# Kernel tuning notes

Hardware: AMD Instinct MI355X
Metric: run time of the kernel (lower is better)

Reference implementation:

```python
import jax, jax.numpy as jnp
import numpy as np
import math
from jax import lax

L = 16
T = 2 ** 14          # hash table size (power of 2 -> uint32 arithmetic is exact mod T)
F_DIM = 2
N_MIN, N_MAX = 16, 512
_B = math.exp((math.log(N_MAX) - math.log(N_MIN)) / (L - 1))
NS = [int(N_MIN * _B ** i) for i in range(L)]
PRIME = np.uint32(2654435761)


def setup_inputs() -> dict:
    key = jax.random.key(0)
    k1, k2 = jax.random.split(key)
    x = jax.random.uniform(k1, (8, 2, 512, 512), dtype=jnp.float32)
    hash_table = jax.random.uniform(k2, (L, T, F_DIM), dtype=jnp.float32) * 2e-4 - 1e-4
    return {"x": x, "hash_table": hash_table}


def reference(x, hash_table):
    b, c, h, w = x.shape
    feats = []
    for i, n in enumerate(NS):
        kh, kw = h // n, w // n
        # max_pool2d(x*n, (kh,kw), stride=1) -> [b, 2, h-kh+1, w-kw+1]
        g = lax.reduce_window(x * n, -jnp.inf, lax.max,
                              (1, 1, kh, kw), (1, 1, 1, 1), 'VALID')
        g = g.astype(jnp.uint32)  # trunc toward zero, values nonneg and small
        # prime-XOR hash; T is a power of two so uint32 wraparound matches int64 math mod T
        idx = (g[:, 0] ^ (g[:, 1] * PRIME)) % np.uint32(T)  # [b, gh, gw]
        f = hash_table[i][idx]                 # gather -> [b, gh, gw, F_DIM]
        f = jnp.transpose(f, (0, 3, 1, 2))     # [b, F_DIM, gh, gw]
        # bilinear upsample (half-pixel centers == align_corners=False)
        f = jax.image.resize(f, (b, F_DIM, h, w), method='bilinear')
        feats.append(f)
    return jnp.concatenate(feats, axis=1)       # [b, L*F_DIM, h, w]
```

## Files before the change

kernel.cpp:

```cpp
#include <hip/hip_runtime.h>
#include <stdint.h>

#define NLVL 16
#define TSIZE 16384
#define HW 512

typedef float vfloat4 __attribute__((ext_vector_type(4)));

__constant__ int c_n[NLVL] = {16,20,25,32,40,50,64,80,101,128,161,203,256,322,406,512};

__device__ __forceinline__ uint32_t pkmax(uint32_t a, uint32_t b) {
    uint32_t r;
    asm("v_pk_max_u16 %0, %1, %2" : "=v"(r) : "v"(a), "v"(b));
    return r;
}

template<int K>
__device__ __forceinline__ void do_tile(
        const int lvl, const int b, const int tx0, const int ty0,
        const float* __restrict__ x, const float* __restrict__ table,
        float* __restrict__ out, uint32_t* lds) {
    constexpr int gh = 513 - K;
    constexpr float s = (float)gh * (1.0f / 512.0f);
    const float nf = (float)c_n[lvl];
    const int tid = threadIdx.x;

    const float* xb0 = x + (size_t)b * 2 * HW * HW;
    const float* xb1 = xb0 + HW * HW;
    const float2* tb = (const float2*)table + (size_t)lvl * TSIZE;
    float* ob = out + ((size_t)b * 32 + lvl * 2) * HW * HW;

    uint32_t* V   = lds;
    float2*  feat = (float2*)(lds + 33 * 68);

    const int gy_base = (int)floorf(((float)ty0 + 0.5f) * s - 0.5f);
    const int gx_base = (int)floorf(((float)tx0 + 0.5f) * s - 0.5f);
    const int rmin = max(gy_base, 0);
    const int cmin = max(gx_base, 0);

    {
        const int wv = __builtin_amdgcn_readfirstlane(tid >> 6);
        const int c  = tid & 63;
        const int r0 = 8 * wv;
        const int xx = min(cmin + c, HW - 1);
        const int ybase = rmin + r0;
        uint32_t e[K + 8];
#pragma unroll
        for (int t = 0; t < K + 8; ++t) {
            const int yy = min(ybase + t, HW - 1);
            const float v0 = (xb0 + yy * HW)[xx];
            const float v1 = (xb1 + yy * HW)[xx];
            e[t] = (uint32_t)(v0 * nf) | ((uint32_t)(v1 * nf) << 16);
        }
        uint32_t o[9];
        if constexpr (K >= 10) {
            uint32_t sfx[9];
            sfx[8] = e[8];
#pragma unroll
            for (int t = 7; t >= 0; --t) sfx[t] = pkmax(e[t], sfx[t + 1]);
            uint32_t run = e[9];
#pragma unroll
            for (int m = 9; m <= K + 7; ++m) {
                if (m > 9) run = pkmax(run, e[m]);
                if (m >= K - 1) o[m - K + 1] = pkmax(sfx[m - K + 1], run);
            }
        } else {
#pragma unroll
            for (int i = 0; i < 9; ++i) {
                uint32_t m = e[i];
#pragma unroll
                for (int t = 1; t < K; ++t) m = pkmax(m, e[i + t]);
                o[i] = m;
            }
        }
        const int vb = r0 * 68 + c;
#pragma unroll
        for (int t = 0; t < 9; ++t) V[vb + t * 68] = o[t];
    }
    __syncthreads();

    if (tid < 99) {
        const int i = tid / 3, g = tid % 3;
        constexpr int NE  = 12 + K - 1;
        constexpr int NCH = (NE + 3) >> 2;
        uint32_t f[NCH * 4];
        const uint4* rp = (const uint4*)(V + i * 68 + 12 * g);
#pragma unroll
        for (int cc = 0; cc < NCH; ++cc) {
            const uint4 q = rp[cc];
            f[4*cc] = q.x; f[4*cc+1] = q.y; f[4*cc+2] = q.z; f[4*cc+3] = q.w;
        }
        uint32_t wm[12];
        if constexpr (K >= 13) {
            uint32_t sfx[12];
            sfx[11] = f[11];
#pragma unroll
            for (int d = 10; d >= 0; --d) sfx[d] = pkmax(f[d], sfx[d + 1]);
            uint32_t run = f[12];
#pragma unroll
            for (int m = 12; m <= K + 10; ++m) {
                if (m > 12) run = pkmax(run, f[m]);
                if (m >= K - 1) wm[m - K + 1] = pkmax(sfx[m - K + 1], run);
            }
        } else {
#pragma unroll
            for (int d = 0; d < 12; ++d) {
                uint32_t m = f[d];
#pragma unroll
                for (int t = 1; t < K; ++t) m = pkmax(m, f[d + t]);
                wm[d] = m;
            }
        }
#pragma unroll
        for (int d = 0; d < 12; ++d) {
            const int j = 12 * g + d;
            if (j < 33) {
                const uint32_t m = wm[d];
                const uint32_t idx = ((m & 0xFFFFu) ^ ((m >> 16) * 2654435761u)) & (TSIZE - 1);
                feat[i * 34 + j] = tb[idx];
            }
        }
    }
    __syncthreads();

    const int bty = tid >> 5, btx = tid & 31;
    const int xo = tx0 + btx;
    const float sxf = ((float)xo + 0.5f) * s - 0.5f;
    const float fxf = floorf(sxf);
    const float wx = sxf - fxf;
    const int x0i = (int)fxf;
    const int jx0 = min(max(x0i, 0), gh - 1) - cmin;
    const int jx1 = min(max(x0i + 1, 0), gh - 1) - cmin;
    for (int oy = bty; oy < 32; oy += 8) {
        const int y = ty0 + oy;
        const float syf = ((float)y + 0.5f) * s - 0.5f;
        const float fyf = floorf(syf);
        const float wy = syf - fyf;
        const int y0i = (int)fyf;
        const int iy0 = min(max(y0i, 0), gh - 1) - rmin;
        const int iy1 = min(max(y0i + 1, 0), gh - 1) - rmin;
        const float2 f00 = feat[iy0 * 34 + jx0], f01 = feat[iy0 * 34 + jx1];
        const float2 f10 = feat[iy1 * 34 + jx0], f11 = feat[iy1 * 34 + jx1];
        const float w11 = wy * wx;
        const float w10 = wy - w11;
        const float w01 = wx - w11;
        const float w00 = 1.0f - wy - wx + w11;
        const float c0 = f00.x * w00 + f01.x * w01 + f10.x * w10 + f11.x * w11;
        const float c1 = f00.y * w00 + f01.y * w01 + f10.y * w10 + f11.y * w11;
        const size_t o = (size_t)y * HW + xo;
        __builtin_nontemporal_store(c0, &ob[o]);
        __builtin_nontemporal_store(c1, &ob[o + (size_t)HW * HW]);
    }
}

__device__ __forceinline__ void identity3(
        const int b, const int tx0, const int ty0,
        const float* __restrict__ x, const float* __restrict__ table,
        float* __restrict__ out) {
    const int tid = threadIdx.x;
    const int oy = tid >> 3, xo = tx0 + (tid & 7) * 4;
    const int y = ty0 + oy;
    const float* xb0 = x + (size_t)b * 2 * HW * HW;
    const float* xb1 = xb0 + HW * HW;
    const float4 v0 = *(const float4*)&xb0[y * HW + xo];
    const float4 v1 = *(const float4*)&xb1[y * HW + xo];
    const size_t o = (size_t)y * HW + xo;
#pragma unroll
    for (int li = 0; li < 3; ++li) {
        const int lvl = 13 + li;
        const float nf = (float)c_n[13 + li];
        const float2* tb = (const float2*)table + (size_t)lvl * TSIZE;
        float* ob = out + ((size_t)b * 32 + lvl * 2) * HW * HW;
        const uint32_t i0 = (((uint32_t)(v0.x * nf)) ^ (((uint32_t)(v1.x * nf)) * 2654435761u)) & (TSIZE - 1);
        const uint32_t i1 = (((uint32_t)(v0.y * nf)) ^ (((uint32_t)(v1.y * nf)) * 2654435761u)) & (TSIZE - 1);
        const uint32_t i2 = (((uint32_t)(v0.z * nf)) ^ (((uint32_t)(v1.z * nf)) * 2654435761u)) & (TSIZE - 1);
        const uint32_t i3 = (((uint32_t)(v0.w * nf)) ^ (((uint32_t)(v1.w * nf)) * 2654435761u)) & (TSIZE - 1);
        const float2 f0 = tb[i0], f1 = tb[i1], f2 = tb[i2], f3 = tb[i3];
        const vfloat4 o0 = (vfloat4){f0.x, f1.x, f2.x, f3.x};
        const vfloat4 o1 = (vfloat4){f0.y, f1.y, f2.y, f3.y};
        __builtin_nontemporal_store(o0, (vfloat4*)&ob[o]);
        __builtin_nontemporal_store(o1, (vfloat4*)&ob[o + (size_t)HW * HW]);
    }
}

__global__ __launch_bounds__(256) void fused_kernel(
        const float* __restrict__ x, const float* __restrict__ table,
        float* __restrict__ out) {
    __shared__ __align__(16) uint32_t lds[33 * 68 + 33 * 34 * 2];

    const int bid  = blockIdx.x;
    const int b    = bid & 7;
    const int tile = (bid >> 3) & 255;
    const int grp  = bid >> 11;
    const int tx0  = (tile & 15) * 32;
    const int ty0  = (tile >> 4) * 32;

    switch (grp) {
        case 0: do_tile<32>( 0, b, tx0, ty0, x, table, out, lds);
                do_tile<25>( 1, b, tx0, ty0, x, table, out, lds); break;
        case 1: do_tile<20>( 2, b, tx0, ty0, x, table, out, lds);
                do_tile<16>( 3, b, tx0, ty0, x, table, out, lds); break;
        case 2: do_tile<12>( 4, b, tx0, ty0, x, table, out, lds);
                do_tile<10>( 5, b, tx0, ty0, x, table, out, lds); break;
        case 3: do_tile< 8>( 6, b, tx0, ty0, x, table, out, lds);
                do_tile< 6>( 7, b, tx0, ty0, x, table, out, lds); break;
        case 4: do_tile< 5>( 8, b, tx0, ty0, x, table, out, lds);
                do_tile< 4>( 9, b, tx0, ty0, x, table, out, lds); break;
        case 5: do_tile< 3>(10, b, tx0, ty0, x, table, out, lds);
                do_tile< 2>(11, b, tx0, ty0, x, table, out, lds); break;
        case 6: do_tile< 2>(12, b, tx0, ty0, x, table, out, lds); break;
        default: identity3(b, tx0, ty0, x, table, out); break;
    }
}

extern "C" void kernel_launch(void* const* d_in, const int* in_sizes, int n_in,
                              void* d_out, int out_size, void* d_ws, size_t ws_size,
                              hipStream_t stream) {
    const float* x     = (const float*)d_in[0];
    const float* table = (const float*)d_in[1];
    float* out         = (float*)d_out;
    (void)d_ws; (void)ws_size;

    fused_kernel<<<dim3(8 * 256 * 8), dim3(256), 0, stream>>>(x, table, out);
}
```

Baseline: 111.7 us.

## Share input column loads between paired pyramid levels in one pass

Paired levels now read the input column strip once and quantize it at both scales, computing the vertical window max for both levels from the same registers. The second level's partial results go into a separate LDS buffer, offset by the row and column difference between the two levels' tile origins. This removes a second pass of global loads per pair. In exchange it uses more registers (two element arrays, extra outputs) and more LDS, which may lower occupancy.

```diff
diff --git a/kernel.cpp b/kernel.cpp
--- a/kernel.cpp
+++ b/kernel.cpp
@@ -15,70 +15,36 @@
     return r;
 }
 
+template<int KK, int P, int NE>
+__device__ __forceinline__ void winmaxNU(const uint32_t (&e)[NE], uint32_t (&o)[P]) {
+    static_assert(NE >= P + KK - 1, "window overrun");
+    if constexpr (KK > P) {
+        uint32_t sfx[P];
+        sfx[P - 1] = e[P - 1];
+#pragma unroll
+        for (int t = P - 2; t >= 0; --t) sfx[t] = pkmax(e[t], sfx[t + 1]);
+        uint32_t run = e[P];
+#pragma unroll
+        for (int m = P; m <= P + KK - 2; ++m) {
+            if (m > P) run = pkmax(run, e[m]);
+            const int j = m - KK + 1;
+            if (j >= 0 && j < P) o[j] = pkmax(sfx[j], run);
+        }
+    } else {
+#pragma unroll
+        for (int i = 0; i < P; ++i) {
+            uint32_t m = e[i];
+#pragma unroll
+            for (int t = 1; t < KK; ++t) m = pkmax(m, e[i + t]);
+            o[i] = m;
+        }
+    }
+}
+
 template<int K>
-__device__ __forceinline__ void do_tile(
-        const int lvl, const int b, const int tx0, const int ty0,
-        const float* __restrict__ x, const float* __restrict__ table,
-        float* __restrict__ out, uint32_t* lds) {
-    constexpr int gh = 513 - K;
-    constexpr float s = (float)gh * (1.0f / 512.0f);
-    const float nf = (float)c_n[lvl];
-    const int tid = threadIdx.x;
-
-    const float* xb0 = x + (size_t)b * 2 * HW * HW;
-    const float* xb1 = xb0 + HW * HW;
-    const float2* tb = (const float2*)table + (size_t)lvl * TSIZE;
-    float* ob = out + ((size_t)b * 32 + lvl * 2) * HW * HW;
-
-    uint32_t* V   = lds;
-    float2*  feat = (float2*)(lds + 33 * 68);
-
-    const int gy_base = (int)floorf(((float)ty0 + 0.5f) * s - 0.5f);
-    const int gx_base = (int)floorf(((float)tx0 + 0.5f) * s - 0.5f);
-    const int rmin = max(gy_base, 0);
-    const int cmin = max(gx_base, 0);
-
-    {
-        const int wv = __builtin_amdgcn_readfirstlane(tid >> 6);
-        const int c  = tid & 63;
-        const int r0 = 8 * wv;
-        const int xx = min(cmin + c, HW - 1);
-        const int ybase = rmin + r0;
-        uint32_t e[K + 8];
-#pragma unroll
-        for (int t = 0; t < K + 8; ++t) {
-            const int yy = min(ybase + t, HW - 1);
-            const float v0 = (xb0 + yy * HW)[xx];
-            const float v1 = (xb1 + yy * HW)[xx];
-            e[t] = (uint32_t)(v0 * nf) | ((uint32_t)(v1 * nf) << 16);
-        }
-        uint32_t o[9];
-        if constexpr (K >= 10) {
-            uint32_t sfx[9];
-            sfx[8] = e[8];
-#pragma unroll
-            for (int t = 7; t >= 0; --t) sfx[t] = pkmax(e[t], sfx[t + 1]);
-            uint32_t run = e[9];
-#pragma unroll
-            for (int m = 9; m <= K + 7; ++m) {
-                if (m > 9) run = pkmax(run, e[m]);
-                if (m >= K - 1) o[m - K + 1] = pkmax(sfx[m - K + 1], run);
-            }
-        } else {
-#pragma unroll
-            for (int i = 0; i < 9; ++i) {
-                uint32_t m = e[i];
-#pragma unroll
-                for (int t = 1; t < K; ++t) m = pkmax(m, e[i + t]);
-                o[i] = m;
-            }
-        }
-        const int vb = r0 * 68 + c;
-#pragma unroll
-        for (int t = 0; t < 9; ++t) V[vb + t * 68] = o[t];
-    }
-    __syncthreads();
-
+__device__ __forceinline__ void phaseB(const uint32_t* __restrict__ V,
+                                       float2* __restrict__ feat,
+                                       const float2* __restrict__ tb, const int tid) {
     if (tid < 99) {
         const int i = tid / 3, g = tid % 3;
         constexpr int NE  = 12 + K - 1;
@@ -91,26 +57,7 @@
             f[4*cc] = q.x; f[4*cc+1] = q.y; f[4*cc+2] = q.z; f[4*cc+3] = q.w;
         }
         uint32_t wm[12];
-        if constexpr (K >= 13) {
-            uint32_t sfx[12];
-            sfx[11] = f[11];
-#pragma unroll
-            for (int d = 10; d >= 0; --d) sfx[d] = pkmax(f[d], sfx[d + 1]);
-            uint32_t run = f[12];
-#pragma unroll
-            for (int m = 12; m <= K + 10; ++m) {
-                if (m > 12) run = pkmax(run, f[m]);
-                if (m >= K - 1) wm[m - K + 1] = pkmax(sfx[m - K + 1], run);
-            }
-        } else {
-#pragma unroll
-            for (int d = 0; d < 12; ++d) {
-                uint32_t m = f[d];
-#pragma unroll
-                for (int t = 1; t < K; ++t) m = pkmax(m, f[d + t]);
-                wm[d] = m;
-            }
-        }
+        winmaxNU<K, 12, NCH * 4>(f, wm);
 #pragma unroll
         for (int d = 0; d < 12; ++d) {
             const int j = 12 * g + d;
@@ -121,8 +68,15 @@
             }
         }
     }
-    __syncthreads();
-
+}
+
+template<int K>
+__device__ __forceinline__ void phaseC(const float2* __restrict__ feat,
+                                       float* __restrict__ ob,
+                                       const int rmin, const int cmin,
+                                       const int tx0, const int ty0, const int tid) {
+    constexpr int gh = 513 - K;
+    constexpr float s = (float)gh * (1.0f / 512.0f);
     const int bty = tid >> 5, btx = tid & 31;
     const int xo = tx0 + btx;
     const float sxf = ((float)xo + 0.5f) * s - 0.5f;
@@ -153,6 +107,114 @@
     }
 }
 
+template<int K1, int K2>
+__device__ __forceinline__ void do_pair(
+        const int l1, const int l2, const int b, const int tx0, const int ty0,
+        const float* __restrict__ x, const float* __restrict__ table,
+        float* __restrict__ out, uint32_t* lds) {
+    constexpr float s1 = (float)(513 - K1) * (1.0f / 512.0f);
+    constexpr float s2 = (float)(513 - K2) * (1.0f / 512.0f);
+    const float nf1 = (float)c_n[l1], nf2 = (float)c_n[l2];
+    const int tid = threadIdx.x;
+
+    const float* xb0 = x + (size_t)b * 2 * HW * HW;
+    const float* xb1 = xb0 + HW * HW;
+
+    uint32_t* V1  = lds;
+    uint32_t* V2  = lds + 2244;
+    float2*  feat = (float2*)(lds + 4488);
+
+    const int rmin1 = max((int)floorf(((float)ty0 + 0.5f) * s1 - 0.5f), 0);
+    const int cmin1 = max((int)floorf(((float)tx0 + 0.5f) * s1 - 0.5f), 0);
+    const int rmin2 = max((int)floorf(((float)ty0 + 0.5f) * s2 - 0.5f), 0);
+    const int cmin2 = max((int)floorf(((float)tx0 + 0.5f) * s2 - 0.5f), 0);
+    const int dr = rmin2 - rmin1;
+    const int dc = cmin2 - cmin1;
+
+    {
+        const int wv = __builtin_amdgcn_readfirstlane(tid >> 6);
+        const int c  = tid & 63;
+        const int r0 = 8 * wv;
+        const int xx = min(cmin1 + c, HW - 1);
+        const int ybase = rmin1 + r0;
+        uint32_t eA[K1 + 8], eB[K1 + 8];
+#pragma unroll
+        for (int t = 0; t < K1 + 8; ++t) {
+            const int yy = min(ybase + t, HW - 1);
+            const float v0 = (xb0 + yy * HW)[xx];
+            const float v1 = (xb1 + yy * HW)[xx];
+            eA[t] = (uint32_t)(v0 * nf1) | ((uint32_t)(v1 * nf1) << 16);
+            eB[t] = (uint32_t)(v0 * nf2) | ((uint32_t)(v1 * nf2) << 16);
+        }
+        uint32_t o1[9];
+        winmaxNU<K1, 9, K1 + 8>(eA, o1);
+        const int vb = r0 * 68 + c;
+#pragma unroll
+        for (int t = 0; t < 9; ++t) V1[vb + t * 68] = o1[t];
+
+        constexpr int P2 = K1 - K2 + 9;
+        uint32_t o2[P2];
+        winmaxNU<K2, P2, K1 + 8>(eB, o2);
+        const int c2 = c - dc;
+#pragma unroll
+        for (int j = 0; j < P2; ++j) {
+            const int i2 = r0 + j - dr;
+            if (i2 >= 0 && i2 <= 32 && c2 >= 0)
+                V2[i2 * 68 + c2] = o2[j];
+        }
+    }
+    __syncthreads();
+
+    phaseB<K1>(V1, feat, (const float2*)table + (size_t)l1 * TSIZE, tid);
+    __syncthreads();
+    phaseC<K1>(feat, out + ((size_t)b * 32 + l1 * 2) * HW * HW, rmin1, cmin1, tx0, ty0, tid);
+    __syncthreads();
+    phaseB<K2>(V2, feat, (const float2*)table + (size_t)l2 * TSIZE, tid);
+    __syncthreads();
+    phaseC<K2>(feat, out + ((size_t)b * 32 + l2 * 2) * HW * HW, rmin2, cmin2, tx0, ty0, tid);
+}
+
+template<int K>
+__device__ __forceinline__ void do_tile(
+        const int lvl, const int b, const int tx0, const int ty0,
+        const float* __restrict__ x, const float* __restrict__ table,
+        float* __restrict__ out, uint32_t* lds) {
+    constexpr float s = (float)(513 - K) * (1.0f / 512.0f);
+    const float nf = (float)c_n[lvl];
+    const int tid = threadIdx.x;
+    const float* xb0 = x + (size_t)b * 2 * HW * HW;
+    const float* xb1 = xb0 + HW * HW;
+    uint32_t* V   = lds;
+    float2*  feat = (float2*)(lds + 2244);
+
+    const int rmin = max((int)floorf(((float)ty0 + 0.5f) * s - 0.5f), 0);
+    const int cmin = max((int)floorf(((float)tx0 + 0.5f) * s - 0.5f), 0);
+    {
+        const int wv = __builtin_amdgcn_readfirstlane(tid >> 6);
+        const int c  = tid & 63;
+        const int r0 = 8 * wv;
+        const int xx = min(cmin + c, HW - 1);
+        const int ybase = rmin + r0;
+        uint32_t e[K + 8];
+#pragma unroll
+        for (int t = 0; t < K + 8; ++t) {
+            const int yy = min(ybase + t, HW - 1);
+            const float v0 = (xb0 + yy * HW)[xx];
+            const float v1 = (xb1 + yy * HW)[xx];
+            e[t] = (uint32_t)(v0 * nf) | ((uint32_t)(v1 * nf) << 16);
+        }
+        uint32_t o[9];
+        winmaxNU<K, 9, K + 8>(e, o);
+        const int vb = r0 * 68 + c;
+#pragma unroll
+        for (int t = 0; t < 9; ++t) V[vb + t * 68] = o[t];
+    }
+    __syncthreads();
+    phaseB<K>(V, feat, (const float2*)table + (size_t)lvl * TSIZE, tid);
+    __syncthreads();
+    phaseC<K>(feat, out + ((size_t)b * 32 + lvl * 2) * HW * HW, rmin, cmin, tx0, ty0, tid);
+}
+
 __device__ __forceinline__ void identity3(
         const int b, const int tx0, const int ty0,
         const float* __restrict__ x, const float* __restrict__ table,
@@ -186,7 +248,7 @@
 __global__ __launch_bounds__(256) void fused_kernel(
         const float* __restrict__ x, const float* __restrict__ table,
         float* __restrict__ out) {
-    __shared__ __align__(16) uint32_t lds[33 * 68 + 33 * 34 * 2];
+    __shared__ __align__(16) uint32_t lds[6732];
 
     const int bid  = blockIdx.x;
     const int b    = bid & 7;
@@ -196,18 +258,12 @@
     const int ty0  = (tile >> 4) * 32;
 
     switch (grp) {
-        case 0: do_tile<32>( 0, b, tx0, ty0, x, table, out, lds);
-                do_tile<25>( 1, b, tx0, ty0, x, table, out, lds); break;
-        case 1: do_tile<20>( 2, b, tx0, ty0, x, table, out, lds);
-                do_tile<16>( 3, b, tx0, ty0, x, table, out, lds); break;
-        case 2: do_tile<12>( 4, b, tx0, ty0, x, table, out, lds);
-                do_tile<10>( 5, b, tx0, ty0, x, table, out, lds); break;
-        case 3: do_tile< 8>( 6, b, tx0, ty0, x, table, out, lds);
-                do_tile< 6>( 7, b, tx0, ty0, x, table, out, lds); break;
-        case 4: do_tile< 5>( 8, b, tx0, ty0, x, table, out, lds);
-                do_tile< 4>( 9, b, tx0, ty0, x, table, out, lds); break;
-        case 5: do_tile< 3>(10, b, tx0, ty0, x, table, out, lds);
-                do_tile< 2>(11, b, tx0, ty0, x, table, out, lds); break;
+        case 0: do_pair<32,25>( 0,  1, b, tx0, ty0, x, table, out, lds); break;
+        case 1: do_pair<20,16>( 2,  3, b, tx0, ty0, x, table, out, lds); break;
+        case 2: do_pair<12,10>( 4,  5, b, tx0, ty0, x, table, out, lds); break;
+        case 3: do_pair< 8, 6>( 6,  7, b, tx0, ty0, x, table, out, lds); break;
+        case 4: do_pair< 5, 4>( 8,  9, b, tx0, ty0, x, table, out, lds); break;
+        case 5: do_pair< 3, 2>(10, 11, b, tx0, ty0, x, table, out, lds); break;
         case 6: do_tile< 2>(12, b, tx0, ty0, x, table, out, lds); break;
         default: identity3(b, tx0, ty0, x, table, out); break;
     }
```

Measured after the change: 106.0 us. 5.1% less time.
